# Performance work log

Measured on AMD Instinct MI355X. Metric: run time of the kernel, lower is better.

## Reference

```python
import jax, jax.numpy as jnp
import numpy as np

B, S, D = 4, 2048, 512   # batch, seq_len, hidden_size
H, HD = 1, 512           # num_heads (must be 1 given the view), head_size
ALPHA, BW, A = 2.0, 512.0, 0.5
EPS = 1e-12              # F.normalize / cdist-grad stabilizer


def setup_inputs() -> dict:
    key = jax.random.key(0)
    ks = jax.random.split(key, 7)
    s = 1.0 / np.sqrt(D)  # keep q,k,v at unit scale like trained weights
    return {
        "x": jax.random.normal(ks[0], (B, S, D), jnp.float32),
        "Wq": jax.random.normal(ks[1], (HD, D), jnp.float32) * s,
        "bq": jax.random.normal(ks[2], (HD,), jnp.float32) * 0.01,
        "Wk": jax.random.normal(ks[3], (HD, D), jnp.float32) * s,
        "bk": jax.random.normal(ks[4], (HD,), jnp.float32) * 0.01,
        "Wv": jax.random.normal(ks[5], (HD, D), jnp.float32) * s,
        "bv": jax.random.normal(ks[6], (HD,), jnp.float32) * 0.01,
    }


def reference(x, Wq, bq, Wk, bk, Wv, bv):
    # projections, then (B, H, S, HD)
    q = (x @ Wq.T + bq).reshape(B, S, H, HD).transpose(0, 2, 1, 3)
    k = (x @ Wk.T + bk).reshape(B, S, H, HD).transpose(0, 2, 1, 3)
    v = (x @ Wv.T + bv).reshape(B, S, H, HD).transpose(0, 2, 1, 3)

    # torch.cdist(q, k, p=2): pairwise Euclidean distance, shape (B, H, S, S)
    sq = ((q * q).sum(-1)[..., :, None]
          + (k * k).sum(-1)[..., None, :]
          - 2.0 * jnp.einsum('bhsd,bhtd->bhst', q, k))
    g_dist = jnp.sqrt(jnp.maximum(sq, EPS))

    # alpha >= 2 branch: exp(-(g / sqrt(bw))**(alpha/(alpha-1)))
    attn_score = jnp.exp(-(g_dist / jnp.sqrt(BW)) ** (ALPHA / (ALPHA - 1.0)))

    # bistochastic (Sinkhorn-like) renormalization, a > 0 branch
    N_R = attn_score.sum(-1)   # row sums  (B, H, S)
    N_C = attn_score.sum(-2)   # col sums  (B, H, S)
    K_tilde = (N_R ** (-A))[..., :, None] * attn_score * (N_C ** (-A))[..., None, :]

    # F.normalize(K_tilde, p=1, dim=3); entries are nonnegative so |.| == .
    probs = K_tilde / jnp.maximum(K_tilde.sum(-1, keepdims=True), EPS)

    # dropout prob = 0.0 -> identity
    out = jnp.einsum('bhst,bhtd->bhsd', probs, v)
    return out, probs
```

## Files before the change

kernel.cpp:

```cpp
#include <hip/hip_runtime.h>
#include <hip/hip_bf16.h>

typedef short short8 __attribute__((ext_vector_type(8)));
typedef short short4v __attribute__((ext_vector_type(4)));
typedef float f32x4 __attribute__((ext_vector_type(4)));

#define S_LEN 2048
#define DIM   512
#define NBATCH 4

typedef unsigned short ushort_t;

__device__ __forceinline__ float b2f(unsigned short u) {
    union { unsigned u; float f; } x; x.u = ((unsigned)u) << 16; return x.f;
}
__device__ __forceinline__ unsigned short f2b(float f) {
    union { float f; unsigned u; } x; x.f = f;
    unsigned r = x.u + 0x7FFFu + ((x.u >> 16) & 1u);
    return (unsigned short)(r >> 16);
}
__device__ __forceinline__ float wave_sum(float v) {
    #pragma unroll
    for (int off = 32; off > 0; off >>= 1) v += __shfl_xor(v, off, 64);
    return v;
}
__device__ __forceinline__ void gld16(const void* g, void* l) {
    __builtin_amdgcn_global_load_lds(
        (const __attribute__((address_space(1))) unsigned int*)g,
        (__attribute__((address_space(3))) unsigned int*)l, 16, 0, 0);
}

__global__ void convert_kernel(const float* __restrict__ x,
                               const float* __restrict__ Wq,
                               const float* __restrict__ Wk,
                               const float* __restrict__ Wv,
                               ushort_t* __restrict__ xb,
                               ushort_t* __restrict__ Wb)
{
    const int blk = blockIdx.x;
    const float* src;
    ushort_t* dst;
    size_t off;
    if (blk < 2048) {
        src = x; dst = xb; off = (size_t)blk * 2048;
    } else {
        int w = (blk - 2048) >> 7;
        int r = (blk - 2048) & 127;
        src = (w == 0) ? Wq : (w == 1) ? Wk : Wv;
        dst = Wb + (size_t)w * DIM * DIM;
        off = (size_t)r * 2048;
    }
    size_t i = off + (size_t)threadIdx.x * 8;
    f32x4 a = *(const f32x4*)&src[i];
    f32x4 c = *(const f32x4*)&src[i + 4];
    short8 o;
    #pragma unroll
    for (int e = 0; e < 4; e++) {
        o[e]     = (short)f2b(a[e]);
        o[4 + e] = (short)f2b(c[e]);
    }
    *(short8*)&dst[i] = o;
}

__global__ void proj_kernel(
    const ushort_t* __restrict__ xb,
    const ushort_t* __restrict__ Wb,
    const float* __restrict__ bq, const float* __restrict__ bk,
    const float* __restrict__ bv,
    ushort_t* __restrict__ Q, ushort_t* __restrict__ Kp,
    ushort_t* __restrict__ Vt)
{
    __shared__ __align__(16) ushort_t As[128 * 32];
    __shared__ __align__(16) ushort_t Bs[128 * 32];
    const int z = blockIdx.z;
    const ushort_t* A  = xb;
    const ushort_t* Bt = Wb + (size_t)z * DIM * DIM;
    const float* bias = (z == 0) ? bq : (z == 1) ? bk : bv;

    const int bm0 = blockIdx.x * 128, bn0 = blockIdx.y * 128;
    const int tid = threadIdx.x;
    const int lane = tid & 63, wave = tid >> 6;
    const int wm = wave >> 1, wn = wave & 1;
    const int quad = lane >> 4;
    const int mrow = wm * 64 + (lane & 15);
    const int ncol = wn * 64 + (lane & 15);
    f32x4 acc[4][4] = {};

    for (int k0 = 0; k0 < DIM; k0 += 32) {
        __syncthreads();
        #pragma unroll
        for (int u = 0; u < 2; u++) {
            int f = u * 256 + tid;
            int row = f >> 2, c4 = (f & 3) ^ ((row >> 1) & 3);
            gld16(&A[(size_t)(bm0 + row) * DIM + k0 + c4 * 8],
                  &As[(u * 256 + wave * 64) * 8]);
        }
        #pragma unroll
        for (int u = 0; u < 2; u++) {
            int f = u * 256 + tid;
            int row = f >> 2, c4 = (f & 3) ^ ((row >> 1) & 3);
            gld16(&Bt[(size_t)(bn0 + row) * DIM + k0 + c4 * 8],
                  &Bs[(u * 256 + wave * 64) * 8]);
        }
        __syncthreads();

        short8 af[4], bf[4];
        #pragma unroll
        for (int i = 0; i < 4; i++) {
            int row = mrow + 16 * i;
            af[i] = *(const short8*)&As[row * 32 + (quad ^ ((row >> 1) & 3)) * 8];
        }
        #pragma unroll
        for (int j = 0; j < 4; j++) {
            int row = ncol + 16 * j;
            bf[j] = *(const short8*)&Bs[row * 32 + (quad ^ ((row >> 1) & 3)) * 8];
        }
        #pragma unroll
        for (int i = 0; i < 4; i++)
            #pragma unroll
            for (int j = 0; j < 4; j++)
                acc[i][j] = __builtin_amdgcn_mfma_f32_16x16x32_bf16(
                    af[i], bf[j], acc[i][j], 0, 0, 0);
    }

    #pragma unroll
    for (int j = 0; j < 4; j++) {
        int gcol = bn0 + wn * 64 + 16 * j + (lane & 15);
        float bb = bias[gcol];
        #pragma unroll
        for (int i = 0; i < 4; i++)
            #pragma unroll
            for (int r = 0; r < 4; r++) {
                int grow = bm0 + wm * 64 + 16 * i + quad * 4 + r;
                ushort_t o = f2b(acc[i][j][r] + bb);
                if (z == 0)      Q[(size_t)grow * DIM + gcol] = o;
                else if (z == 1) Kp[(size_t)grow * DIM + gcol] = o;
                else {
                    int bb2 = grow >> 11, s = grow & 2047;
                    Vt[((size_t)bb2 * DIM + gcol) * S_LEN + s] = o;
                }
            }
    }
}

__global__ void norms_kernel(const ushort_t* __restrict__ Q,
                             const ushort_t* __restrict__ Kp,
                             float* __restrict__ nq, float* __restrict__ nk)
{
    const int wave = threadIdx.x >> 6, lane = threadIdx.x & 63;
    const int row = blockIdx.x * 4 + wave;
    const ushort_t* src = (blockIdx.y == 0) ? Q : Kp;
    float* dst = (blockIdx.y == 0) ? nq : nk;
    short8 v = *(const short8*)&src[(size_t)row * DIM + lane * 8];
    float s = 0.f;
    #pragma unroll
    for (int e = 0; e < 8; e++) { float f = b2f((ushort_t)v[e]); s += f * f; }
    s = wave_sum(s);
    if (lane == 0) dst[row] = s;
}

__global__ void score_kernel(const ushort_t* __restrict__ Q,
                             const ushort_t* __restrict__ Kp,
                             const float* __restrict__ nq,
                             const float* __restrict__ nk,
                             ushort_t* __restrict__ attnb,
                             float* __restrict__ NC)
{
    __shared__ __align__(16) ushort_t As[128 * 32];
    __shared__ __align__(16) ushort_t Bs[128 * 32];
    const int b = blockIdx.z;
    const ushort_t* A  = Q  + (size_t)b * S_LEN * DIM;
    const ushort_t* Bt = Kp + (size_t)b * S_LEN * DIM;
    const int bm0 = blockIdx.x * 128, bn0 = blockIdx.y * 128;
    const int tid = threadIdx.x;
    const int lane = tid & 63, wave = tid >> 6;
    const int wm = wave >> 1, wn = wave & 1;
    const int quad = lane >> 4;
    const int mrow = wm * 64 + (lane & 15);
    const int ncol = wn * 64 + (lane & 15);
    f32x4 acc[4][4] = {};

    for (int k0 = 0; k0 < DIM; k0 += 32) {
        __syncthreads();
        #pragma unroll
        for (int u = 0; u < 2; u++) {
            int f = u * 256 + tid;
            int row = f >> 2, c4 = (f & 3) ^ ((row >> 1) & 3);
            gld16(&A[(size_t)(bm0 + row) * DIM + k0 + c4 * 8],
                  &As[(u * 256 + wave * 64) * 8]);
        }
        #pragma unroll
        for (int u = 0; u < 2; u++) {
            int f = u * 256 + tid;
            int row = f >> 2, c4 = (f & 3) ^ ((row >> 1) & 3);
            gld16(&Bt[(size_t)(bn0 + row) * DIM + k0 + c4 * 8],
                  &Bs[(u * 256 + wave * 64) * 8]);
        }
        __syncthreads();

        short8 af[4], bf[4];
        #pragma unroll
        for (int i = 0; i < 4; i++) {
            int row = mrow + 16 * i;
            af[i] = *(const short8*)&As[row * 32 + (quad ^ ((row >> 1) & 3)) * 8];
        }
        #pragma unroll
        for (int j = 0; j < 4; j++) {
            int row = ncol + 16 * j;
            bf[j] = *(const short8*)&Bs[row * 32 + (quad ^ ((row >> 1) & 3)) * 8];
        }
        #pragma unroll
        for (int i = 0; i < 4; i++)
            #pragma unroll
            for (int j = 0; j < 4; j++)
                acc[i][j] = __builtin_amdgcn_mfma_f32_16x16x32_bf16(
                    af[i], bf[j], acc[i][j], 0, 0, 0);
    }

    ushort_t* ob = attnb + (size_t)b * S_LEN * S_LEN;
    float nqv[16], nkv[4];
    #pragma unroll
    for (int i = 0; i < 4; i++)
        #pragma unroll
        for (int r = 0; r < 4; r++)
            nqv[i * 4 + r] = nq[b * S_LEN + bm0 + wm * 64 + 16 * i + quad * 4 + r];
    #pragma unroll
    for (int j = 0; j < 4; j++)
        nkv[j] = nk[b * S_LEN + bn0 + wn * 64 + 16 * j + (lane & 15)];

    float cp[4] = {0.f, 0.f, 0.f, 0.f};
    #pragma unroll
    for (int i = 0; i < 4; i++)
        #pragma unroll
        for (int j = 0; j < 4; j++)
            #pragma unroll
            for (int r = 0; r < 4; r++) {
                int grow = bm0 + wm * 64 + 16 * i + quad * 4 + r;
                int gcol = bn0 + wn * 64 + 16 * j + (lane & 15);
                float sq = nqv[i * 4 + r] + nkv[j] - 2.0f * acc[i][j][r];
                sq = fmaxf(sq, 1e-12f);
                ushort_t ub = f2b(__expf(sq * (-1.0f / 512.0f)));
                ob[(size_t)grow * S_LEN + gcol] = ub;
                cp[j] += b2f(ub);
            }
    #pragma unroll
    for (int j = 0; j < 4; j++) {
        float v = cp[j];
        v += __shfl_xor(v, 16, 64);
        v += __shfl_xor(v, 32, 64);
        if (quad == 0) {
            int gcol = bn0 + wn * 64 + 16 * j + (lane & 15);
            atomicAdd(&NC[b * S_LEN + gcol], v);
        }
    }
}

__global__ void finalize_c_kernel(const float* __restrict__ NC, float* __restrict__ c)
{
    int i = blockIdx.x * 256 + threadIdx.x;
    c[i] = 1.0f / sqrtf(NC[i]);
}

__global__ void scale_vt_kernel(ushort_t* __restrict__ Vt,
                                const float* __restrict__ cc)
{
    size_t idx = ((size_t)blockIdx.x * 256 + threadIdx.x) * 8;
    int s0 = (int)(idx & 2047);
    int b  = (int)(idx >> 20);
    const float* cb = cc + (b << 11);
    short8 v = *(short8*)&Vt[idx];
    #pragma unroll
    for (int e = 0; e < 8; e++)
        v[e] = (short)f2b(b2f((ushort_t)v[e]) * cb[s0 + e]);
    *(short8*)&Vt[idx] = v;
}

__global__ void rowsumprobs_kernel(const ushort_t* __restrict__ attnb,
                                   const float* __restrict__ cc,
                                   float* __restrict__ probs,
                                   float* __restrict__ rr)
{
    __shared__ float red[4];
    const int s = blockIdx.x, b = blockIdx.y;
    const size_t R = (size_t)b * S_LEN + s;
    const ushort_t* row = attnb + R * S_LEN;
    const float* cb = cc + (b << 11);
    const int t = threadIdx.x * 8;
    const int wave = threadIdx.x >> 6, lane = threadIdx.x & 63;

    short8 av = *(const short8*)&row[t];
    float pv[8], acc = 0.f;
    #pragma unroll
    for (int e = 0; e < 8; e++) { pv[e] = b2f((ushort_t)av[e]) * cb[t + e]; acc += pv[e]; }
    acc = wave_sum(acc);
    if (lane == 0) red[wave] = acc;
    __syncthreads();
    float rs = 1.0f / (red[0] + red[1] + red[2] + red[3]);

    float* prow = probs + R * S_LEN;
    f32x4 o0, o1;
    #pragma unroll
    for (int e = 0; e < 4; e++) { o0[e] = pv[e] * rs; o1[e] = pv[4 + e] * rs; }
    *(f32x4*)&prow[t] = o0;
    *(f32x4*)&prow[t + 4] = o1;
    if (threadIdx.x == 0) rr[R] = rs;
}

__global__ void out_gemm_kernel(const ushort_t* __restrict__ attnb,
                                const ushort_t* __restrict__ Vtc,
                                const float* __restrict__ rr,
                                float* __restrict__ outp)
{
    __shared__ __align__(16) ushort_t As[128 * 32];
    __shared__ __align__(16) ushort_t Bs[64 * 32];
    const int b = blockIdx.z;
    const ushort_t* A  = attnb + (size_t)b * S_LEN * S_LEN;
    const ushort_t* Bt = Vtc + (size_t)b * DIM * S_LEN;
    const int bm0 = blockIdx.x * 128, bn0 = blockIdx.y * 64;
    const int tid = threadIdx.x;
    const int lane = tid & 63, wave = tid >> 6;
    const int wm = wave >> 2, wn = wave & 3;
    const int quad = lane >> 4;
    const int mrow = wm * 64 + (lane & 15);
    const int ncol = wn * 16 + (lane & 15);
    f32x4 acc[4] = {};

    for (int k0 = 0; k0 < S_LEN; k0 += 32) {
        __syncthreads();
        {
            int f = tid;
            int row = f >> 2, c4 = (f & 3) ^ ((row >> 1) & 3);
            gld16(&A[(size_t)(bm0 + row) * S_LEN + k0 + c4 * 8],
                  &As[(wave * 64) * 8]);
        }
        if (wave < 4) {
            int f = wave * 64 + lane;
            int row = f >> 2, c4 = (f & 3) ^ ((row >> 1) & 3);
            gld16(&Bt[(size_t)(bn0 + row) * S_LEN + k0 + c4 * 8],
                  &Bs[(wave * 64) * 8]);
        }
        __syncthreads();

        short8 af[4], bf;
        #pragma unroll
        for (int i = 0; i < 4; i++) {
            int row = mrow + 16 * i;
            af[i] = *(const short8*)&As[row * 32 + (quad ^ ((row >> 1) & 3)) * 8];
        }
        {
            int row = ncol;
            bf = *(const short8*)&Bs[row * 32 + (quad ^ ((row >> 1) & 3)) * 8];
        }
        #pragma unroll
        for (int i = 0; i < 4; i++)
            acc[i] = __builtin_amdgcn_mfma_f32_16x16x32_bf16(af[i], bf, acc[i], 0, 0, 0);
    }

    float* C = outp + (size_t)b * S_LEN * DIM;
    const int gcol = bn0 + wn * 16 + (lane & 15);
    #pragma unroll
    for (int i = 0; i < 4; i++)
        #pragma unroll
        for (int r = 0; r < 4; r++) {
            int grow = bm0 + wm * 64 + 16 * i + quad * 4 + r;
            float rs = rr[b * S_LEN + grow];
            C[(size_t)grow * DIM + gcol] = acc[i][r] * rs;
        }
}

extern "C" void kernel_launch(void* const* d_in, const int* in_sizes, int n_in,
                              void* d_out, int out_size, void* d_ws, size_t ws_size,
                              hipStream_t stream)
{
    const float* x  = (const float*)d_in[0];
    const float* Wq = (const float*)d_in[1];
    const float* bq = (const float*)d_in[2];
    const float* Wk = (const float*)d_in[3];
    const float* bk = (const float*)d_in[4];
    const float* Wv = (const float*)d_in[5];
    const float* bv = (const float*)d_in[6];

    float* out   = (float*)d_out;
    float* probs = out + (size_t)NBATCH * S_LEN * DIM;

    ushort_t* Qb = (ushort_t*)d_out;
    ushort_t* Kb = Qb + (size_t)8192 * DIM;
    ushort_t* xb = (ushort_t*)probs;
    ushort_t* Wb = xb + (size_t)8192 * DIM;
    ushort_t* Vt    = (ushort_t*)d_ws;
    ushort_t* attnb = Vt + (size_t)NBATCH * DIM * S_LEN;
    float* nq = (float*)(attnb + (size_t)NBATCH * S_LEN * S_LEN);
    float* nk = nq + 8192;
    float* NC = nk + 8192;
    float* cc = NC + 8192;
    float* rr = cc + 8192;

    hipMemsetAsync(NC, 0, 8192 * sizeof(float), stream);

    convert_kernel<<<2432, 256, 0, stream>>>(x, Wq, Wk, Wv, xb, Wb);
    proj_kernel<<<dim3(64, 4, 3), 256, 0, stream>>>(xb, Wb, bq, bk, bv,
                                                    Qb, Kb, Vt);
    norms_kernel<<<dim3(2048, 2), 256, 0, stream>>>(Qb, Kb, nq, nk);
    score_kernel<<<dim3(16, 16, NBATCH), 256, 0, stream>>>(Qb, Kb, nq, nk,
                                                           attnb, NC);
    finalize_c_kernel<<<32, 256, 0, stream>>>(NC, cc);
    scale_vt_kernel<<<2048, 256, 0, stream>>>(Vt, cc);
    rowsumprobs_kernel<<<dim3(S_LEN, NBATCH), 256, 0, stream>>>(attnb, cc,
                                                                probs, rr);
    out_gemm_kernel<<<dim3(16, 8, NBATCH), 512, 0, stream>>>(attnb, Vt, rr, out);
}
```

Before: 220.6 us.

## Enlarge out-GEMM tile, fuse column-norm rsqrt, vectorize V-transpose stores

The output GEMM now computes a 128x128 tile with 256 threads, each wave holding a 4x4 MFMA accumulator block instead of 4x1. This raises operand reuse from LDS and halves the number of times the attention matrix is re-read. The separate finalize kernel is removed and rsqrt of the column sums is computed inline in the consumers. The projection epilogue for V writes 4 contiguous bf16 values per store into the transposed layout instead of scattered scalar stores. The costs are more registers per thread and fewer blocks (256) for the GEMM.

```diff
diff --git a/kernel.cpp b/kernel.cpp
--- a/kernel.cpp
+++ b/kernel.cpp
@@ -123,23 +123,35 @@
                     af[i], bf[j], acc[i][j], 0, 0, 0);
     }
 
-    #pragma unroll
-    for (int j = 0; j < 4; j++) {
-        int gcol = bn0 + wn * 64 + 16 * j + (lane & 15);
-        float bb = bias[gcol];
-        #pragma unroll
-        for (int i = 0; i < 4; i++)
-            #pragma unroll
-            for (int r = 0; r < 4; r++) {
-                int grow = bm0 + wm * 64 + 16 * i + quad * 4 + r;
-                ushort_t o = f2b(acc[i][j][r] + bb);
-                if (z == 0)      Q[(size_t)grow * DIM + gcol] = o;
-                else if (z == 1) Kp[(size_t)grow * DIM + gcol] = o;
-                else {
-                    int bb2 = grow >> 11, s = grow & 2047;
-                    Vt[((size_t)bb2 * DIM + gcol) * S_LEN + s] = o;
+    if (z < 2) {
+        ushort_t* O = (z == 0) ? Q : Kp;
+        #pragma unroll
+        for (int j = 0; j < 4; j++) {
+            int gcol = bn0 + wn * 64 + 16 * j + (lane & 15);
+            float bb = bias[gcol];
+            #pragma unroll
+            for (int i = 0; i < 4; i++)
+                #pragma unroll
+                for (int r = 0; r < 4; r++) {
+                    int grow = bm0 + wm * 64 + 16 * i + quad * 4 + r;
+                    O[(size_t)grow * DIM + gcol] = f2b(acc[i][j][r] + bb);
                 }
+        }
+    } else {
+        #pragma unroll
+        for (int j = 0; j < 4; j++) {
+            int gcol = bn0 + wn * 64 + 16 * j + (lane & 15);
+            float bb = bias[gcol];
+            #pragma unroll
+            for (int i = 0; i < 4; i++) {
+                int grow0 = bm0 + wm * 64 + 16 * i + quad * 4;
+                int bb2 = grow0 >> 11, s = grow0 & 2047;
+                short4v o4;
+                #pragma unroll
+                for (int r = 0; r < 4; r++) o4[r] = (short)f2b(acc[i][j][r] + bb);
+                *(short4v*)&Vt[((size_t)bb2 * DIM + gcol) * S_LEN + s] = o4;
             }
+        }
     }
 }
 
@@ -255,28 +267,22 @@
     }
 }
 
-__global__ void finalize_c_kernel(const float* __restrict__ NC, float* __restrict__ c)
-{
-    int i = blockIdx.x * 256 + threadIdx.x;
-    c[i] = 1.0f / sqrtf(NC[i]);
-}
-
 __global__ void scale_vt_kernel(ushort_t* __restrict__ Vt,
-                                const float* __restrict__ cc)
+                                const float* __restrict__ NC)
 {
     size_t idx = ((size_t)blockIdx.x * 256 + threadIdx.x) * 8;
     int s0 = (int)(idx & 2047);
     int b  = (int)(idx >> 20);
-    const float* cb = cc + (b << 11);
+    const float* cb = NC + (b << 11);
     short8 v = *(short8*)&Vt[idx];
     #pragma unroll
     for (int e = 0; e < 8; e++)
-        v[e] = (short)f2b(b2f((ushort_t)v[e]) * cb[s0 + e]);
+        v[e] = (short)f2b(b2f((ushort_t)v[e]) * rsqrtf(cb[s0 + e]));
     *(short8*)&Vt[idx] = v;
 }
 
 __global__ void rowsumprobs_kernel(const ushort_t* __restrict__ attnb,
-                                   const float* __restrict__ cc,
+                                   const float* __restrict__ NC,
                                    float* __restrict__ probs,
                                    float* __restrict__ rr)
 {
@@ -284,14 +290,17 @@
     const int s = blockIdx.x, b = blockIdx.y;
     const size_t R = (size_t)b * S_LEN + s;
     const ushort_t* row = attnb + R * S_LEN;
-    const float* cb = cc + (b << 11);
+    const float* cb = NC + (b << 11);
     const int t = threadIdx.x * 8;
     const int wave = threadIdx.x >> 6, lane = threadIdx.x & 63;
 
     short8 av = *(const short8*)&row[t];
     float pv[8], acc = 0.f;
     #pragma unroll
-    for (int e = 0; e < 8; e++) { pv[e] = b2f((ushort_t)av[e]) * cb[t + e]; acc += pv[e]; }
+    for (int e = 0; e < 8; e++) {
+        pv[e] = b2f((ushort_t)av[e]) * rsqrtf(cb[t + e]);
+        acc += pv[e];
+    }
     acc = wave_sum(acc);
     if (lane == 0) red[wave] = acc;
     __syncthreads();
@@ -312,60 +321,74 @@
                                 float* __restrict__ outp)
 {
     __shared__ __align__(16) ushort_t As[128 * 32];
-    __shared__ __align__(16) ushort_t Bs[64 * 32];
+    __shared__ __align__(16) ushort_t Bs[128 * 32];
     const int b = blockIdx.z;
     const ushort_t* A  = attnb + (size_t)b * S_LEN * S_LEN;
     const ushort_t* Bt = Vtc + (size_t)b * DIM * S_LEN;
-    const int bm0 = blockIdx.x * 128, bn0 = blockIdx.y * 64;
+    const int bm0 = blockIdx.x * 128, bn0 = blockIdx.y * 128;
     const int tid = threadIdx.x;
     const int lane = tid & 63, wave = tid >> 6;
-    const int wm = wave >> 2, wn = wave & 3;
+    const int wm = wave >> 1, wn = wave & 1;
     const int quad = lane >> 4;
     const int mrow = wm * 64 + (lane & 15);
-    const int ncol = wn * 16 + (lane & 15);
-    f32x4 acc[4] = {};
+    const int ncol = wn * 64 + (lane & 15);
+    f32x4 acc[4][4] = {};
 
     for (int k0 = 0; k0 < S_LEN; k0 += 32) {
         __syncthreads();
-        {
-            int f = tid;
+        #pragma unroll
+        for (int u = 0; u < 2; u++) {
+            int f = u * 256 + tid;
             int row = f >> 2, c4 = (f & 3) ^ ((row >> 1) & 3);
             gld16(&A[(size_t)(bm0 + row) * S_LEN + k0 + c4 * 8],
-                  &As[(wave * 64) * 8]);
-        }
-        if (wave < 4) {
-            int f = wave * 64 + lane;
+                  &As[(u * 256 + wave * 64) * 8]);
+        }
+        #pragma unroll
+        for (int u = 0; u < 2; u++) {
+            int f = u * 256 + tid;
             int row = f >> 2, c4 = (f & 3) ^ ((row >> 1) & 3);
             gld16(&Bt[(size_t)(bn0 + row) * S_LEN + k0 + c4 * 8],
-                  &Bs[(wave * 64) * 8]);
-        }
-        __syncthreads();
-
-        short8 af[4], bf;
+                  &Bs[(u * 256 + wave * 64) * 8]);
+        }
+        __syncthreads();
+
+        short8 af[4], bf[4];
         #pragma unroll
         for (int i = 0; i < 4; i++) {
             int row = mrow + 16 * i;
             af[i] = *(const short8*)&As[row * 32 + (quad ^ ((row >> 1) & 3)) * 8];
         }
-        {
-            int row = ncol;
-            bf = *(const short8*)&Bs[row * 32 + (quad ^ ((row >> 1) & 3)) * 8];
+        #pragma unroll
+        for (int j = 0; j < 4; j++) {
+            int row = ncol + 16 * j;
+            bf[j] = *(const short8*)&Bs[row * 32 + (quad ^ ((row >> 1) & 3)) * 8];
         }
         #pragma unroll
         for (int i = 0; i < 4; i++)
-            acc[i] = __builtin_amdgcn_mfma_f32_16x16x32_bf16(af[i], bf, acc[i], 0, 0, 0);
+            #pragma unroll
+            for (int j = 0; j < 4; j++)
+                acc[i][j] = __builtin_amdgcn_mfma_f32_16x16x32_bf16(
+                    af[i], bf[j], acc[i][j], 0, 0, 0);
     }
 
     float* C = outp + (size_t)b * S_LEN * DIM;
-    const int gcol = bn0 + wn * 16 + (lane & 15);
+    float rv[16];
     #pragma unroll
     for (int i = 0; i < 4; i++)
         #pragma unroll
-        for (int r = 0; r < 4; r++) {
-            int grow = bm0 + wm * 64 + 16 * i + quad * 4 + r;
-            float rs = rr[b * S_LEN + grow];
-            C[(size_t)grow * DIM + gcol] = acc[i][r] * rs;
-        }
+        for (int r = 0; r < 4; r++)
+            rv[i * 4 + r] = rr[b * S_LEN + bm0 + wm * 64 + 16 * i + quad * 4 + r];
+    #pragma unroll
+    for (int j = 0; j < 4; j++) {
+        int gcol = bn0 + wn * 64 + 16 * j + (lane & 15);
+        #pragma unroll
+        for (int i = 0; i < 4; i++)
+            #pragma unroll
+            for (int r = 0; r < 4; r++) {
+                int grow = bm0 + wm * 64 + 16 * i + quad * 4 + r;
+                C[(size_t)grow * DIM + gcol] = acc[i][j][r] * rv[i * 4 + r];
+            }
+    }
 }
 
 extern "C" void kernel_launch(void* const* d_in, const int* in_sizes, int n_in,
@@ -403,9 +426,8 @@
     norms_kernel<<<dim3(2048, 2), 256, 0, stream>>>(Qb, Kb, nq, nk);
     score_kernel<<<dim3(16, 16, NBATCH), 256, 0, stream>>>(Qb, Kb, nq, nk,
                                                            attnb, NC);
-    finalize_c_kernel<<<32, 256, 0, stream>>>(NC, cc);
-    scale_vt_kernel<<<2048, 256, 0, stream>>>(Vt, cc);
-    rowsumprobs_kernel<<<dim3(S_LEN, NBATCH), 256, 0, stream>>>(attnb, cc,
+    scale_vt_kernel<<<2048, 256, 0, stream>>>(Vt, NC);
+    rowsumprobs_kernel<<<dim3(S_LEN, NBATCH), 256, 0, stream>>>(attnb, NC,
                                                                 probs, rr);
-    out_gemm_kernel<<<dim3(16, 8, NBATCH), 512, 0, stream>>>(attnb, Vt, rr, out);
-}
+    out_gemm_kernel<<<dim3(16, 4, NBATCH), 256, 0, stream>>>(attnb, Vt, rr, out);
+}
```

Result: faster. 211.3 us (-4.2%).
